# Optimization experiments

Hardware: AMD Instinct MI355X
Metric: run time of the kernel (lower is better)

## Reference

```python
import jax, jax.numpy as jnp
import numpy as np

H, HKV, D, HID = 12, 2, 128, 1536
NGROUPS = H // HKV  # 6


def rotate_half(x):
    half = x.shape[-1] // 2
    x1, x2 = x[..., :half], x[..., half:]
    return jnp.concatenate([-x2, x1], axis=-1)


def setup_inputs() -> dict:
    key = jax.random.key(0)
    k0, k1, k2, k3 = jax.random.split(key, 4)
    B, S = 4, 2048
    NSLOTS = 16384
    x = jax.random.normal(k0, (B, S, HID), jnp.float32)
    # RoPE tables (concat-style, matches RoPE class): theta=1e6
    inv_freq = 1.0 / (1000000.0 ** (np.arange(0, D, 2, dtype=np.float64) / D))
    ang = np.outer(np.arange(S, dtype=np.float64), inv_freq)  # (S, D/2)
    cos_t = np.concatenate([np.cos(ang), np.cos(ang)], axis=-1).astype(np.float32)
    sin_t = np.concatenate([np.sin(ang), np.sin(ang)], axis=-1).astype(np.float32)
    cos = jnp.broadcast_to(jnp.asarray(cos_t)[None], (B, S, D))
    sin = jnp.broadcast_to(jnp.asarray(sin_t)[None], (B, S, D))
    kv_cache_k = jnp.zeros((NSLOTS, HKV, D), jnp.float32)
    kv_cache_v = jnp.zeros((NSLOTS, HKV, D), jnp.float32)
    slot_mapping = jnp.arange(B * S, dtype=jnp.int32)  # unique, in-range slots
    Wqkv = 0.02 * jax.random.normal(k1, (H * D + 2 * HKV * D, HID), jnp.float32)
    bqkv = 0.02 * jax.random.normal(k2, (H * D + 2 * HKV * D,), jnp.float32)
    Wo = 0.02 * jax.random.normal(k3, (HID, HID), jnp.float32)
    return {"x": x, "cos": cos, "sin": sin, "kv_cache_k": kv_cache_k,
            "kv_cache_v": kv_cache_v, "slot_mapping": slot_mapping,
            "Wqkv": Wqkv, "bqkv": bqkv, "Wo": Wo, "is_prefill": 1}


def reference(x, cos, sin, kv_cache_k, kv_cache_v, slot_mapping, Wqkv, bqkv, Wo, is_prefill):
    B, S, _ = x.shape
    qkv = x @ Wqkv.T + bqkv  # (B,S,2048)
    q_size, k_size = H * D, HKV * D
    q = qkv[..., :q_size].reshape(B, S, H, D)
    k = qkv[..., q_size:q_size + k_size].reshape(B, S, HKV, D)
    v = qkv[..., q_size + k_size:].reshape(B, S, HKV, D)
    # fused RoPE (concat-style rotate_half)
    cb, sb = cos[:, :, None, :], sin[:, :, None, :]
    q = q * cb + rotate_half(q) * sb
    k = k * cb + rotate_half(k) * sb
    # paged KV-cache store (scatter by slot)
    k_flat = k.reshape(-1, HKV, D)
    v_flat = v.reshape(-1, HKV, D)
    kc = kv_cache_k.at[slot_mapping].set(k_flat)
    vc = kv_cache_v.at[slot_mapping].set(v_flat)
    # prefill: causal GQA SDPA
    kr = jnp.repeat(k, NGROUPS, axis=2)  # (B,S,H,D)
    vr = jnp.repeat(v, NGROUPS, axis=2)
    scale = 1.0 / jnp.sqrt(jnp.float32(D))
    scores = jnp.einsum('bqhd,bkhd->bhqk', q, kr) * scale  # (B,H,S,S)
    causal = jnp.tril(jnp.ones((S, S), bool))
    scores = jnp.where(causal, scores, jnp.float32(-1e30))
    attn = jax.nn.softmax(scores, axis=-1)
    out = jnp.einsum('bhqk,bkhd->bqhd', attn, vr).reshape(B, S, HID)
    out = out @ Wo.T
    return out, kc, vc
```

## Files before the change

kernel.cpp:

```cpp
#include <hip/hip_runtime.h>
#include <hip/hip_bf16.h>
#include <stdint.h>

typedef __attribute__((ext_vector_type(8))) __bf16 bf16x8;
typedef __attribute__((ext_vector_type(4))) float f32x4;

__device__ __forceinline__ float bf2f(unsigned short u) {
  unsigned int x = ((unsigned int)u) << 16;
  float f; __builtin_memcpy(&f, &x, 4); return f;
}
__device__ __forceinline__ unsigned short f2bf(float f) {
  unsigned int x; __builtin_memcpy(&x, &f, 4);
  unsigned int r = x + 0x7fffu + ((x >> 16) & 1u);
  return (unsigned short)(r >> 16);
}
__device__ __forceinline__ unsigned int pk2(float a, float b) {
  __hip_bfloat162 h = __float22bfloat162_rn(float2{a, b});
  unsigned int u; __builtin_memcpy(&u, &h, 4); return u;
}
__device__ __forceinline__ uint4 cvt8(const float* src) {
  float4 a = *(const float4*)src;
  float4 b = *(const float4*)(src + 4);
  uint4 r;
  r.x = pk2(a.x, a.y); r.y = pk2(a.z, a.w);
  r.z = pk2(b.x, b.y); r.w = pk2(b.z, b.w);
  return r;
}

__device__ __forceinline__ void gload_lds16(const unsigned short* g, unsigned short* l) {
  __builtin_amdgcn_global_load_lds(
      (const __attribute__((address_space(1))) void*)g,
      (__attribute__((address_space(3))) void*)l, 16, 0, 0);
}

__global__ __launch_bounds__(256) void cvt_all(const float* __restrict__ x,
                                               const float* __restrict__ wqkv,
                                               const float* __restrict__ wo,
                                               unsigned short* __restrict__ xb,
                                               unsigned short* __restrict__ wqkvb,
                                               unsigned short* __restrict__ wob) {
  long i = ((long)blockIdx.x * 256 + threadIdx.x) * 8;
  if (i < 12582912) { *(uint4*)(xb + i) = cvt8(x + i); return; }
  i -= 12582912;
  if (i < 3145728) { *(uint4*)(wqkvb + i) = cvt8(wqkv + i); return; }
  i -= 3145728;
  *(uint4*)(wob + i) = cvt8(wo + i);
}

template <bool OUT_F32, bool HAS_BIAS>
__global__ __launch_bounds__(256) void gemm_bt(const unsigned short* __restrict__ A,
                                               const unsigned short* __restrict__ W,
                                               const float* __restrict__ bias,
                                               void* __restrict__ Cv,
                                               int M, int N, int K) {
  __shared__ __align__(16) unsigned short sA[128 * 32];
  __shared__ __align__(16) unsigned short sB[128 * 32];
  const int tid = threadIdx.x;
  const int lane = tid & 63;
  const int w = tid >> 6;
  const long m0 = (long)blockIdx.y * 128;
  const long n0 = (long)blockIdx.x * 128;
  const int wm = (w >> 1) * 64;
  const int wn = (w & 1) * 64;
  const int fr = lane & 15, fq = lane >> 4;

  const int srow = w * 16 + (lane >> 2);
  const int scol = (lane & 3) * 8;
  const unsigned short* Ag = A + m0 * K + (long)srow * K + scol;
  const unsigned short* Wg = W + n0 * K + (long)srow * K + scol;
  const long rstep = 64L * K;
  unsigned short* sAw = sA + w * 512;
  unsigned short* sBw = sB + w * 512;

  f32x4 acc[4][4];
#pragma unroll
  for (int i = 0; i < 4; ++i)
#pragma unroll
    for (int j = 0; j < 4; ++j) acc[i][j] = f32x4{0.f, 0.f, 0.f, 0.f};

  for (int k0 = 0; k0 < K; k0 += 32) {
    __syncthreads();
    gload_lds16(Ag + k0,         sAw);
    gload_lds16(Ag + rstep + k0, sAw + 2048);
    gload_lds16(Wg + k0,         sBw);
    gload_lds16(Wg + rstep + k0, sBw + 2048);
    __syncthreads();
    bf16x8 af[4], bfr[4];
#pragma unroll
    for (int t = 0; t < 4; ++t) {
      af[t]  = *(const bf16x8*)&sA[(wm + t * 16 + fr) * 32 + fq * 8];
      bfr[t] = *(const bf16x8*)&sB[(wn + t * 16 + fr) * 32 + fq * 8];
    }
#pragma unroll
    for (int mt = 0; mt < 4; ++mt)
#pragma unroll
      for (int nt = 0; nt < 4; ++nt)
        acc[mt][nt] = __builtin_amdgcn_mfma_f32_16x16x32_bf16(af[mt], bfr[nt], acc[mt][nt], 0, 0, 0);
  }

#pragma unroll
  for (int nt = 0; nt < 4; ++nt) {
    long n = n0 + wn + nt * 16 + fr;
    float bv = HAS_BIAS ? bias[n] : 0.f;
#pragma unroll
    for (int mt = 0; mt < 4; ++mt)
#pragma unroll
      for (int r = 0; r < 4; ++r) {
        long m = m0 + wm + mt * 16 + fq * 4 + r;
        float v = acc[mt][nt][r] + bv;
        if (OUT_F32)
          ((float*)Cv)[m * N + n] = v;
        else
          ((unsigned short*)Cv)[m * N + n] = f2bf(v);
      }
  }
}

__global__ __launch_bounds__(256) void rope_scatter(unsigned short* __restrict__ qkv,
                                                    const float* __restrict__ cosb,
                                                    const float* __restrict__ sinb,
                                                    const int* __restrict__ slot_mapping,
                                                    float* __restrict__ kc,
                                                    float* __restrict__ vc,
                                                    unsigned short* __restrict__ vt) {
  const int u = blockIdx.x * 256 + threadIdx.x;
  if (u < 917504) {
    const int m = u / 112;
    const int g = u - m * 112;
    const int head = g >> 3;
    const int d0 = (g & 7) * 8;
    const int slot = slot_mapping[m];
    const size_t base = (size_t)m * 2048;
    const size_t cbase = (size_t)m * 128;
    const int off = head < 12 ? head * 128 : 1536 + (head - 12) * 128;

    union { uint4 q; unsigned short s[8]; } X1, X2, O1, O2;
    X1.q = *(const uint4*)(qkv + base + off + d0);
    X2.q = *(const uint4*)(qkv + base + off + d0 + 64);
    float c1[8], s1[8], c2[8], s2[8];
    *(float4*)&c1[0] = *(const float4*)(cosb + cbase + d0);
    *(float4*)&c1[4] = *(const float4*)(cosb + cbase + d0 + 4);
    *(float4*)&s1[0] = *(const float4*)(sinb + cbase + d0);
    *(float4*)&s1[4] = *(const float4*)(sinb + cbase + d0 + 4);
    *(float4*)&c2[0] = *(const float4*)(cosb + cbase + d0 + 64);
    *(float4*)&c2[4] = *(const float4*)(cosb + cbase + d0 + 68);
    *(float4*)&s2[0] = *(const float4*)(sinb + cbase + d0 + 64);
    *(float4*)&s2[4] = *(const float4*)(sinb + cbase + d0 + 68);

    float o1[8], o2[8];
#pragma unroll
    for (int j = 0; j < 8; ++j) {
      float x1 = bf2f(X1.s[j]), x2 = bf2f(X2.s[j]);
      o1[j] = x1 * c1[j] - x2 * s1[j];
      o2[j] = x2 * c2[j] + x1 * s2[j];
      O1.s[j] = f2bf(o1[j]);
      O2.s[j] = f2bf(o2[j]);
    }
    *(uint4*)(qkv + base + off + d0) = O1.q;
    *(uint4*)(qkv + base + off + d0 + 64) = O2.q;
    if (head >= 12) {
      float* kp = kc + (size_t)slot * 256 + (head - 12) * 128 + d0;
      *(float4*)(kp)      = *(const float4*)&o1[0];
      *(float4*)(kp + 4)  = *(const float4*)&o1[4];
      *(float4*)(kp + 64) = *(const float4*)&o2[0];
      *(float4*)(kp + 68) = *(const float4*)&o2[4];
    }
  } else {
    const int u2 = u - 917504;
    const int m = u2 & 8191;
    const int g = u2 >> 13;
    const int slot = slot_mapping[m];
    union { uint4 q; unsigned short s[8]; } V;
    V.q = *(const uint4*)(qkv + (size_t)m * 2048 + 1792 + g * 8);
    float vo[8];
#pragma unroll
    for (int j = 0; j < 8; ++j) vo[j] = bf2f(V.s[j]);
    float* vp = vc + (size_t)slot * 256 + g * 8;
    *(float4*)(vp)     = *(const float4*)&vo[0];
    *(float4*)(vp + 4) = *(const float4*)&vo[4];
    const int kvh = g >> 4;
    const int d0 = (g & 15) * 8;
    unsigned short* vtp = vt + ((size_t)((m >> 11) * 2 + kvh) * 128 + d0) * 2048 + (m & 2047);
#pragma unroll
    for (int j = 0; j < 8; ++j) vtp[(size_t)j * 2048] = V.s[j];
  }
}

__global__ __launch_bounds__(256) void attn_kernel(const unsigned short* __restrict__ qkv,
                                                   const unsigned short* __restrict__ vt,
                                                   unsigned short* __restrict__ out) {
  const int qbA = blockIdx.x;
  const int qbB = 31 - qbA;
  const int h = blockIdx.y, b = blockIdx.z;
  const int kvh = h / 6;
  __shared__ __align__(16) unsigned short sK[2][64 * 128];
  __shared__ __align__(16) unsigned short sV[2][128 * 64];
  __shared__ __align__(16) unsigned short sP[4][16 * 72];
  const int tid = threadIdx.x, lane = tid & 63, w = tid >> 6;
  const int fr = lane & 15, fq = lane >> 4;
  const float scale = 0.08838834764831845f;
  const float LOG2E = 1.44269504089f;

  bf16x8 qfA[4], qfB[4];
  {
    const unsigned short* qpA =
        qkv + ((size_t)(b * 2048 + qbA * 64 + w * 16 + fr) * 2048 + h * 128 + fq * 8);
    const unsigned short* qpB =
        qkv + ((size_t)(b * 2048 + qbB * 64 + w * 16 + fr) * 2048 + h * 128 + fq * 8);
#pragma unroll
    for (int kt = 0; kt < 4; ++kt) {
      qfA[kt] = *(const bf16x8*)(qpA + kt * 32);
      qfB[kt] = *(const bf16x8*)(qpB + kt * 32);
    }
  }
  float mA = -3.0e38f, lA = 0.f, mB = -3.0e38f, lB = 0.f;
  f32x4 accA[8], accB[8];
#pragma unroll
  for (int i = 0; i < 8; ++i) {
    accA[i] = f32x4{0.f, 0.f, 0.f, 0.f};
    accB[i] = f32x4{0.f, 0.f, 0.f, 0.f};
  }

  auto stage_K = [&](int t, int buf) {
    const size_t tok0 = (size_t)(b * 2048 + t * 64);
#pragma unroll
    for (int i = 0; i < 4; ++i) {
      int c = i * 256 + w * 64 + lane;
      int kv = c >> 4, gp = c & 15;
      int g = gp ^ (kv & 7);
      gload_lds16(qkv + (tok0 + kv) * 2048 + 1536 + kvh * 128 + g * 8,
                  &sK[buf][0] + i * 2048 + w * 512);
    }
  };
  auto stage_VT = [&](int t, int buf) {
    const size_t rowbase = (size_t)((b * 2 + kvh) * 128);
#pragma unroll
    for (int i = 0; i < 4; ++i) {
      int c = i * 256 + w * 64 + lane;
      int d = c >> 3, gp = c & 7;
      int g = gp ^ (d & 7);
      gload_lds16(vt + (rowbase + d) * 2048 + t * 64 + g * 8,
                  &sV[buf][0] + i * 2048 + w * 512);
    }
  };

  auto process = [&](const bf16x8* qf, float& m_i, float& l_i, f32x4* accO,
                     bool diag, int cur) {
    f32x4 s4[4];
#pragma unroll
    for (int ntv = 0; ntv < 4; ++ntv) s4[ntv] = f32x4{0.f, 0.f, 0.f, 0.f};
    __builtin_amdgcn_s_setprio(1);
#pragma unroll
    for (int ntv = 0; ntv < 4; ++ntv) {
      int kvl = ntv * 16 + fr;
      int swz = kvl & 7;
#pragma unroll
      for (int kt = 0; kt < 4; ++kt) {
        bf16x8 kf = *(const bf16x8*)&sK[cur][kvl * 128 + ((kt * 4 + fq) ^ swz) * 8];
        s4[ntv] = __builtin_amdgcn_mfma_f32_16x16x32_bf16(kf, qf[kt], s4[ntv], 0, 0, 0);
      }
    }
    __builtin_amdgcn_s_setprio(0);

    float sc[4][4];
#pragma unroll
    for (int ntv = 0; ntv < 4; ++ntv)
#pragma unroll
      for (int r = 0; r < 4; ++r) {
        float v = s4[ntv][r] * scale;
        if (diag && (ntv * 16 + fq * 4 + r > w * 16 + fr)) v = -1e30f;
        sc[ntv][r] = v;
      }
    float mx = fmaxf(fmaxf(sc[0][0], sc[0][1]), fmaxf(sc[0][2], sc[0][3]));
#pragma unroll
    for (int ntv = 1; ntv < 4; ++ntv)
      mx = fmaxf(mx, fmaxf(fmaxf(sc[ntv][0], sc[ntv][1]), fmaxf(sc[ntv][2], sc[ntv][3])));
    mx = fmaxf(mx, __shfl_xor(mx, 16));
    mx = fmaxf(mx, __shfl_xor(mx, 32));
    float mnew = fmaxf(m_i, mx);
    float al = exp2f((m_i - mnew) * LOG2E);
    float rs = 0.f;
    float pm[4][4];
#pragma unroll
    for (int ntv = 0; ntv < 4; ++ntv)
#pragma unroll
      for (int r = 0; r < 4; ++r) {
        float p = exp2f((sc[ntv][r] - mnew) * LOG2E);
        pm[ntv][r] = p;
        rs += p;
      }
    rs += __shfl_xor(rs, 16);
    rs += __shfl_xor(rs, 32);
    l_i = l_i * al + rs;
    m_i = mnew;
    float al4[4];
#pragma unroll
    for (int r = 0; r < 4; ++r) al4[r] = __shfl(al, fq * 4 + r);
#pragma unroll
    for (int n2 = 0; n2 < 8; ++n2)
#pragma unroll
      for (int r = 0; r < 4; ++r) accO[n2][r] *= al4[r];
#pragma unroll
    for (int ntv = 0; ntv < 4; ++ntv)
#pragma unroll
      for (int r = 0; r < 4; ++r)
        sP[w][fr * 72 + ntv * 16 + fq * 4 + r] = f2bf(pm[ntv][r]);
    __builtin_amdgcn_s_setprio(1);
#pragma unroll
    for (int kt = 0; kt < 2; ++kt) {
      bf16x8 pf = *(const bf16x8*)&sP[w][fr * 72 + kt * 32 + fq * 8];
#pragma unroll
      for (int n2 = 0; n2 < 8; ++n2) {
        int d = n2 * 16 + fr;
        bf16x8 vf = *(const bf16x8*)&sV[cur][d * 64 + (((kt * 4 + fq) ^ (d & 7)) << 3)];
        accO[n2] = __builtin_amdgcn_mfma_f32_16x16x32_bf16(pf, vf, accO[n2], 0, 0, 0);
      }
    }
    __builtin_amdgcn_s_setprio(0);
  };

  stage_K(0, 0);
  stage_VT(0, 0);
  __syncthreads();

  for (int t = 0; t <= qbB; ++t) {
    const int cur = t & 1;
    if (t < qbB) {
      stage_K(t + 1, cur ^ 1);
      stage_VT(t + 1, cur ^ 1);
    }
    if (t <= qbA) process(qfA, mA, lA, accA, t == qbA, cur);
    process(qfB, mB, lB, accB, t == qbB, cur);
    if (t < qbB) __syncthreads();
  }

  auto epilogue = [&](float l_i, const f32x4* accO, int qb) {
    float linv[4];
#pragma unroll
    for (int r = 0; r < 4; ++r) linv[r] = __shfl(l_i, fq * 4 + r);
#pragma unroll
    for (int r = 0; r < 4; ++r) {
      float inv = 1.f / linv[r];
      size_t row = (size_t)(b * 2048 + qb * 64 + w * 16 + fq * 4 + r);
#pragma unroll
      for (int n2 = 0; n2 < 8; ++n2)
        out[row * 1536 + h * 128 + n2 * 16 + fr] = f2bf(accO[n2][r] * inv);
    }
  };
  epilogue(lA, accA, qbA);
  epilogue(lB, accB, qbB);
}

extern "C" void kernel_launch(void* const* d_in, const int* in_sizes, int n_in,
                              void* d_out, int out_size, void* d_ws, size_t ws_size,
                              hipStream_t stream) {
  const float* x    = (const float*)d_in[0];
  const float* cosb = (const float*)d_in[1];
  const float* sinb = (const float*)d_in[2];
  const float* kci  = (const float*)d_in[3];
  const float* vci  = (const float*)d_in[4];
  const int* slot   = (const int*)d_in[5];
  const float* Wqkv = (const float*)d_in[6];
  const float* bqkv = (const float*)d_in[7];
  const float* Wo   = (const float*)d_in[8];

  float* out = (float*)d_out;
  float* kc  = out + (size_t)12582912;
  float* vc  = kc + (size_t)4194304;

  unsigned short* qkv_ws  = (unsigned short*)d_ws;
  unsigned short* attn_ws = qkv_ws + (size_t)16777216;
  unsigned short* xb      = attn_ws;
  unsigned short* wqkvb   = attn_ws + (size_t)12582912;
  unsigned short* wob     = wqkvb + (size_t)3145728;
  unsigned short* vt      = wqkvb;

  hipMemcpyAsync(kc, kci, (size_t)4194304 * 4, hipMemcpyDeviceToDevice, stream);
  hipMemcpyAsync(vc, vci, (size_t)4194304 * 4, hipMemcpyDeviceToDevice, stream);

  cvt_all<<<dim3(8832), 256, 0, stream>>>(x, Wqkv, Wo, xb, wqkvb, wob);
  gemm_bt<false, true><<<dim3(16, 64), 256, 0, stream>>>(
      xb, wqkvb, bqkv, qkv_ws, 8192, 2048, 1536);
  rope_scatter<<<dim3(4608), 256, 0, stream>>>(qkv_ws, cosb, sinb, slot, kc, vc, vt);
  attn_kernel<<<dim3(16, 12, 4), 256, 0, stream>>>(qkv_ws, vt, attn_ws);
  gemm_bt<true, false><<<dim3(12, 64), 256, 0, stream>>>(
      attn_ws, wob, nullptr, out, 8192, 1536, 1536);
}
```

Measured before the change: 545.7 us.

## Interleave two query blocks' QK/softmax/PV and skip rescaling when max barely grows

Splits the attention tile step into separate QK, softmax, P-store and PV stages. When a step has both query blocks, it interleaves them so one block's MFMAs can overlap the other's softmax work. Softmax now uses lazy rescaling: the running max and the accumulator rescale are only updated when some lane's max exceeds the old one by more than 8, which avoids shuffles and multiplies on most steps. It also packs P into 8-byte LDS stores and uses a three-way fmax reduction tree, at the cost of more live registers from holding two score sets at once.

```diff
diff --git a/kernel.cpp b/kernel.cpp
--- a/kernel.cpp
+++ b/kernel.cpp
@@ -17,6 +17,9 @@
 __device__ __forceinline__ unsigned int pk2(float a, float b) {
   __hip_bfloat162 h = __float22bfloat162_rn(float2{a, b});
   unsigned int u; __builtin_memcpy(&u, &h, 4); return u;
+}
+__device__ __forceinline__ float fmax3(float a, float b, float c) {
+  return fmaxf(fmaxf(a, b), c);
 }
 __device__ __forceinline__ uint4 cvt8(const float* src) {
   float4 a = *(const float4*)src;
@@ -244,9 +247,7 @@
     }
   };
 
-  auto process = [&](const bf16x8* qf, float& m_i, float& l_i, f32x4* accO,
-                     bool diag, int cur) {
-    f32x4 s4[4];
+  auto qk = [&](const bf16x8* qf, f32x4* s4, int cur) {
 #pragma unroll
     for (int ntv = 0; ntv < 4; ++ntv) s4[ntv] = f32x4{0.f, 0.f, 0.f, 0.f};
     __builtin_amdgcn_s_setprio(1);
@@ -261,7 +262,10 @@
       }
     }
     __builtin_amdgcn_s_setprio(0);
-
+  };
+
+  auto sm = [&](const f32x4* s4, float& m_i, float& l_i, f32x4* accO,
+                float (&pm)[4][4], bool diag) {
     float sc[4][4];
 #pragma unroll
     for (int ntv = 0; ntv < 4; ++ntv)
@@ -271,40 +275,56 @@
         if (diag && (ntv * 16 + fq * 4 + r > w * 16 + fr)) v = -1e30f;
         sc[ntv][r] = v;
       }
-    float mx = fmaxf(fmaxf(sc[0][0], sc[0][1]), fmaxf(sc[0][2], sc[0][3]));
-#pragma unroll
-    for (int ntv = 1; ntv < 4; ++ntv)
-      mx = fmaxf(mx, fmaxf(fmaxf(sc[ntv][0], sc[ntv][1]), fmaxf(sc[ntv][2], sc[ntv][3])));
+    float p0 = fmax3(sc[0][0], sc[0][1], sc[0][2]);
+    float p1 = fmax3(sc[0][3], sc[1][0], sc[1][1]);
+    float p2 = fmax3(sc[1][2], sc[1][3], sc[2][0]);
+    float p3 = fmax3(sc[2][1], sc[2][2], sc[2][3]);
+    float p4 = fmax3(sc[3][0], sc[3][1], sc[3][2]);
+    float mx = fmaxf(fmax3(p0, p1, p2), fmax3(p3, p4, sc[3][3]));
     mx = fmaxf(mx, __shfl_xor(mx, 16));
     mx = fmaxf(mx, __shfl_xor(mx, 32));
-    float mnew = fmaxf(m_i, mx);
-    float al = exp2f((m_i - mnew) * LOG2E);
-    float rs = 0.f;
-    float pm[4][4];
-#pragma unroll
-    for (int ntv = 0; ntv < 4; ++ntv)
-#pragma unroll
-      for (int r = 0; r < 4; ++r) {
-        float p = exp2f((sc[ntv][r] - mnew) * LOG2E);
-        pm[ntv][r] = p;
-        rs += p;
-      }
+    const bool keep = __all(mx <= m_i + 8.0f);
+    float al = 1.f;
+    if (!keep) {
+      float mnew = fmaxf(m_i, mx);
+      al = exp2f((m_i - mnew) * LOG2E);
+      m_i = mnew;
+    }
+    float rs4[4];
+#pragma unroll
+    for (int ntv = 0; ntv < 4; ++ntv) {
+#pragma unroll
+      for (int r = 0; r < 4; ++r) pm[ntv][r] = exp2f((sc[ntv][r] - m_i) * LOG2E);
+      rs4[ntv] = (pm[ntv][0] + pm[ntv][1]) + (pm[ntv][2] + pm[ntv][3]);
+    }
+    float rs = (rs4[0] + rs4[1]) + (rs4[2] + rs4[3]);
     rs += __shfl_xor(rs, 16);
     rs += __shfl_xor(rs, 32);
-    l_i = l_i * al + rs;
-    m_i = mnew;
-    float al4[4];
-#pragma unroll
-    for (int r = 0; r < 4; ++r) al4[r] = __shfl(al, fq * 4 + r);
-#pragma unroll
-    for (int n2 = 0; n2 < 8; ++n2)
-#pragma unroll
-      for (int r = 0; r < 4; ++r) accO[n2][r] *= al4[r];
-#pragma unroll
-    for (int ntv = 0; ntv < 4; ++ntv)
-#pragma unroll
-      for (int r = 0; r < 4; ++r)
-        sP[w][fr * 72 + ntv * 16 + fq * 4 + r] = f2bf(pm[ntv][r]);
+    if (!keep) {
+      float al4[4];
+#pragma unroll
+      for (int r = 0; r < 4; ++r) al4[r] = __shfl(al, fq * 4 + r);
+#pragma unroll
+      for (int n2 = 0; n2 < 8; ++n2)
+#pragma unroll
+        for (int r = 0; r < 4; ++r) accO[n2][r] *= al4[r];
+      l_i = l_i * al + rs;
+    } else {
+      l_i = l_i + rs;
+    }
+  };
+
+  auto store_p = [&](const float (&pm)[4][4]) {
+#pragma unroll
+    for (int ntv = 0; ntv < 4; ++ntv) {
+      uint2 pkd;
+      pkd.x = pk2(pm[ntv][0], pm[ntv][1]);
+      pkd.y = pk2(pm[ntv][2], pm[ntv][3]);
+      *(uint2*)&sP[w][fr * 72 + ntv * 16 + fq * 4] = pkd;
+    }
+  };
+
+  auto pv = [&](f32x4* accO, int cur) {
     __builtin_amdgcn_s_setprio(1);
 #pragma unroll
     for (int kt = 0; kt < 2; ++kt) {
@@ -329,8 +349,25 @@
       stage_K(t + 1, cur ^ 1);
       stage_VT(t + 1, cur ^ 1);
     }
-    if (t <= qbA) process(qfA, mA, lA, accA, t == qbA, cur);
-    process(qfB, mB, lB, accB, t == qbB, cur);
+    if (t <= qbA) {
+      f32x4 s4A[4], s4B[4];
+      float pmA[4][4], pmB[4][4];
+      qk(qfA, s4A, cur);
+      qk(qfB, s4B, cur);
+      sm(s4A, mA, lA, accA, pmA, t == qbA);
+      store_p(pmA);
+      sm(s4B, mB, lB, accB, pmB, t == qbB);
+      pv(accA, cur);
+      store_p(pmB);
+      pv(accB, cur);
+    } else {
+      f32x4 s4B[4];
+      float pmB[4][4];
+      qk(qfB, s4B, cur);
+      sm(s4B, mB, lB, accB, pmB, t == qbB);
+      store_p(pmB);
+      pv(accB, cur);
+    }
     if (t < qbB) __syncthreads();
   }
 
```

After: 547.9 us. No clear change (+0.4%).
